# Performance work log

Hardware: AMD Instinct MI355X
Metric: run time of the kernel (lower is better)

The kernel has to match this reference:

```python
import jax, jax.numpy as jnp
import numpy as np

B, T, N, H = 256, 128, 128, 256  # batch, window, n_input_series, encoder hidden


def setup_inputs() -> dict:
    key = jax.random.key(0)
    ks = jax.random.split(key, 11)
    s = 0.05
    return {
        "input_data": jax.random.normal(ks[0], (B, T, N), jnp.float32),
        # attn_layer_hidden: Linear(2H -> T)
        "W_ah": jax.random.normal(ks[1], (T, 2 * H), jnp.float32) * s,
        "b_ah": jax.random.normal(ks[2], (T,), jnp.float32) * s,
        # attn_layer_input: Linear(T -> 1)
        "W_ai": jax.random.normal(ks[3], (1, T), jnp.float32) * s,
        "b_ai": jax.random.normal(ks[4], (1,), jnp.float32) * s,
        # attn_layer: Linear(T -> 1)
        "W_a": jax.random.normal(ks[5], (1, T), jnp.float32) * s,
        "b_a": jax.random.normal(ks[6], (1,), jnp.float32) * s,
        # LSTM(N -> H), gate order i,f,g,o (PyTorch)
        "W_ih": jax.random.normal(ks[7], (4 * H, N), jnp.float32) * s,
        "W_hh": jax.random.normal(ks[8], (4 * H, H), jnp.float32) * s,
        "b_ih": jax.random.normal(ks[9], (4 * H,), jnp.float32) * s,
        "b_hh": jax.random.normal(ks[10], (4 * H,), jnp.float32) * s,
    }


def reference(input_data, W_ah, b_ah, W_ai, b_ai, W_a, b_a, W_ih, W_hh, b_ih, b_hh):
    b, t_len, n = input_data.shape
    h_dim = W_hh.shape[1]
    dt = input_data.dtype

    # attn_layer_input part is time-invariant: [B, N] (one scalar per series)
    ipart = jnp.einsum('btn,t->bn', input_data, W_ai[0]) + b_ai[0]

    xs = jnp.swapaxes(input_data, 0, 1)  # [T, B, N]

    def step(carry, x_t):
        h, c = carry  # each [B, H]
        hc = jnp.concatenate([h, c], axis=-1)          # [B, 2H]
        hpart = hc @ W_ah.T + b_ah                      # [B, T]
        z = jnp.tanh(hpart[:, None, :] + ipart[:, :, None])  # [B, N, T]
        score = jnp.einsum('bnt,t->bn', z, W_a[0]) + b_a[0]   # [B, N]
        attn = jax.nn.softmax(score, axis=-1)
        wx = attn * x_t                                 # weighted input [B, N]
        gates = wx @ W_ih.T + b_ih + h @ W_hh.T + b_hh  # [B, 4H]
        i, f, g, o = jnp.split(gates, 4, axis=-1)
        i = jax.nn.sigmoid(i)
        f = jax.nn.sigmoid(f)
        g = jnp.tanh(g)
        o = jax.nn.sigmoid(o)
        c2 = f * c + i * g
        h2 = o * jnp.tanh(c2)
        return (h2, c2), (wx, h2)

    h0 = jnp.zeros((b, h_dim), dt)
    c0 = jnp.zeros((b, h_dim), dt)
    (_, _), (iw, ie) = jax.lax.scan(step, (h0, c0), xs)
    input_weighted = jnp.swapaxes(iw, 0, 1)  # [B, T, N]
    input_encoded = jnp.swapaxes(ie, 0, 1)   # [B, T, H]
    return input_weighted, input_encoded
```

## Files before the change

### kernel.cpp

```cpp
#include <hip/hip_runtime.h>
#include <cstdint>

#define NB 256
#define NT 128
#define NS 128
#define NH 256

#define NTHR 512
#define NWG  256
#define NGRP 64
#define GPW  4
#define GBAT 4
#define UPW  64

#define HC_OFF  0
#define CNT_OFF 131072

typedef _Float16 f16;
typedef _Float16 f16x2 __attribute__((ext_vector_type(2)));
typedef _Float16 f16x8 __attribute__((ext_vector_type(8)));
typedef float    f32x4 __attribute__((ext_vector_type(4)));

#define SAH 528
#define SAG 392

__device__ __forceinline__ f16x2 pk(float a, float b) {
  f16x2 r; r.x = (f16)a; r.y = (f16)b; return r;
}
__device__ __forceinline__ f16x8 pack8(const float* s) {
  float4 v0 = *(const float4*)s, v1 = *(const float4*)(s + 4);
  f16x8 r;
  r[0] = (f16)v0.x; r[1] = (f16)v0.y; r[2] = (f16)v0.z; r[3] = (f16)v0.w;
  r[4] = (f16)v1.x; r[5] = (f16)v1.y; r[6] = (f16)v1.z; r[7] = (f16)v1.w;
  return r;
}
__device__ __forceinline__ void awr(uint32_t* p, uint32_t v) {
  __hip_atomic_store(p, v, __ATOMIC_RELAXED, __HIP_MEMORY_SCOPE_AGENT);
}
__device__ __forceinline__ uint32_t ard(uint32_t* p) {
  return __hip_atomic_load(p, __ATOMIC_RELAXED, __HIP_MEMORY_SCOPE_AGENT);
}
__device__ __forceinline__ void cinc(uint32_t* p) {
  __hip_atomic_fetch_add(p, 1u, __ATOMIC_RELAXED, __HIP_MEMORY_SCOPE_AGENT);
}
__device__ __forceinline__ void cwait(uint32_t* p, uint32_t tgt) {
  while (ard(p) < tgt) __builtin_amdgcn_s_sleep(1);
}

struct __align__(16) Sm {
  f16   wahp[128 * SAH];
  f16   hcp[5 * SAH];
  f16   agxp[5 * SAG];
  float P[128 * 5];
  float scp[4 * 128];
  float gacc[256 * 4];
  float gbias[256];
  float cbuf[256];
  float w2a[128];
  float bah[128];
};

__global__ void enc_init(uint32_t* ws) {
  int i = blockIdx.x * blockDim.x + threadIdx.x;
  if (i < 65536) ws[HC_OFF + i] = 0u;
  if (i < 1024)  ws[CNT_OFF + i] = 0u;
}

__global__ __launch_bounds__(NTHR, 1) void enc_main(
    const float* __restrict__ x,    const float* __restrict__ W_ah,
    const float* __restrict__ b_ah, const float* __restrict__ W_ai,
    const float* __restrict__ b_ai, const float* __restrict__ W_a,
    const float* __restrict__ b_a,  const float* __restrict__ W_ih,
    const float* __restrict__ W_hh, const float* __restrict__ b_ih,
    const float* __restrict__ b_hh, float* __restrict__ out_iw,
    float* __restrict__ out_ie,     uint32_t* __restrict__ ws)
{
  __shared__ Sm sm;
  const int tid  = threadIdx.x;
  const int wg   = blockIdx.x;
  const int xcd  = wg & 7, slot = wg >> 3;
  const int g    = xcd * 8 + (slot >> 2);
  const int gid  = slot & 3;
  const int b0   = g * GBAT;
  const int u0   = gid * UPW;

  const int wv = tid >> 6, ln = tid & 63;
  const int bn = ln & 15, kq = ln >> 4;

  uint32_t* cnt = ws + CNT_OFF + g * 16;

  f16x8 wfrag[2][12];
  #pragma unroll
  for (int tt = 0; tt < 2; ++tt) {
    const int lr = wv * 32 + tt * 16 + bn;
    const int grow = (lr >> 6) * 256 + u0 + (lr & 63);
    #pragma unroll
    for (int kk = 0; kk < 4; ++kk)
      wfrag[tt][kk] = pack8(W_ih + (size_t)grow * NS + kk * 32 + kq * 8);
    #pragma unroll
    for (int kk = 4; kk < 12; ++kk)
      wfrag[tt][kk] = pack8(W_hh + (size_t)grow * NH + (kk - 4) * 32 + kq * 8);
  }

  #pragma unroll
  for (int i = 0; i < 16; ++i) {
    int idx = i * NTHR + tid;
    int r = idx >> 6, c = idx & 63;
    f16x8 v = pack8(W_ah + (size_t)r * 512 + c * 8);
    *(f16x8*)&sm.wahp[(size_t)r * SAH + c * 8] = v;
  }
  if (tid < 256) {
    int grow = (tid >> 6) * 256 + u0 + (tid & 63);
    sm.gbias[tid] = b_ih[grow] + b_hh[grow];
    sm.cbuf[tid] = 0.f;
  }
  if (tid < 128) { sm.w2a[tid] = 2.f * W_a[tid]; sm.bah[tid] = b_ah[tid]; }
  if (tid < 512) sm.hcp[4 * SAH + tid] = (f16)0.f;
  if (tid < 384) sm.agxp[4 * SAG + tid] = (f16)0.f;

  const int n_s = tid & 127, bq_s = tid >> 7;
  float ev;
  {
    const float* xb = x + (size_t)(b0 + bq_s) * NT * NS;
    float a = 0.f;
    #pragma unroll 4
    for (int t = 0; t < NT; ++t) a = fmaf(xb[(size_t)t * NS + n_s], W_ai[t], a);
    ev = __expf(2.f * (a + b_ai[0]));
  }
  float S0;
  { float s = b_a[0]; for (int i = 0; i < 128; ++i) s += W_a[i]; S0 = s; }

  __syncthreads();

  for (int t = 0; t < NT; ++t) {
    const int par = t & 1;
    float xv0 = 0.f, xv1 = 0.f;
    if (wv < 4) {
      const float* xr = x + ((size_t)(b0 + wv) * NT + t) * NS;
      xv0 = xr[ln]; xv1 = xr[ln + 64];
    }
    if (t > 0) {
      if (tid == 0) cwait(cnt, 4u * (uint32_t)t);
      __syncthreads();
    }
    {
      uint32_t* hcb = ws + HC_OFF + ((size_t)par * NGRP + g) * 1024;
      #pragma unroll
      for (int i = 0; i < 2; ++i) {
        int w = i * NTHR + tid;
        uint32_t v = ard(hcb + w);
        f16x2 pv = __builtin_bit_cast(f16x2, v);
        int b = w >> 8, u = w & 255;
        sm.hcp[b * SAH + u] = pv.x;
        sm.hcp[b * SAH + 256 + u] = pv.y;
        sm.agxp[b * SAG + 128 + u] = pv.x;
      }
    }
    __syncthreads();
    {
      f32x4 acc = {0.f, 0.f, 0.f, 0.f};
      const int br = (bn < 4) ? bn : 4;
      #pragma unroll
      for (int kk = 0; kk < 16; ++kk) {
        f16x8 a = *(const f16x8*)&sm.wahp[(size_t)(wv * 16 + bn) * SAH + kk * 32 + kq * 8];
        f16x8 b = *(const f16x8*)&sm.hcp[(size_t)br * SAH + kk * 32 + kq * 8];
        acc = __builtin_amdgcn_mfma_f32_16x16x32_f16(a, b, acc, 0, 0, 0);
      }
      if (bn < 4) {
        const int tp0 = wv * 16 + (ln >> 4) * 4;
        #pragma unroll
        for (int r = 0; r < 4; ++r)
          sm.P[(tp0 + r) * 5 + bn] = __expf(2.f * (acc[r] + sm.bah[tp0 + r]));
      }
    }
    __syncthreads();
    {
      float s = 0.f;
      #pragma unroll 8
      for (int tp = 0; tp < 128; ++tp) {
        float pe = fmaf(sm.P[tp * 5 + bq_s], ev, 1.f);
        s = fmaf(sm.w2a[tp], __builtin_amdgcn_rcpf(pe), s);
      }
      sm.scp[bq_s * 128 + n_s] = S0 - s;
    }
    __syncthreads();
    if (wv < 4) {
      float sA = sm.scp[wv * 128 + ln], sB = sm.scp[wv * 128 + ln + 64];
      float m = fmaxf(sA, sB);
      #pragma unroll
      for (int o = 32; o; o >>= 1) m = fmaxf(m, __shfl_xor(m, o));
      float eA = __expf(sA - m), eB = __expf(sB - m);
      float ss = eA + eB;
      #pragma unroll
      for (int o = 32; o; o >>= 1) ss += __shfl_xor(ss, o);
      float rs = 1.f / ss;
      float wxA = eA * rs * xv0, wxB = eB * rs * xv1;
      sm.agxp[wv * SAG + ln] = (f16)wxA;
      sm.agxp[wv * SAG + ln + 64] = (f16)wxB;
      if (wv == gid) {
        float* ow = out_iw + ((size_t)(b0 + wv) * NT + t) * NS;
        ow[ln] = wxA; ow[ln + 64] = wxB;
      }
    }
    __syncthreads();
    {
      const int br = (bn < 4) ? bn : 4;
      #pragma unroll
      for (int tt = 0; tt < 2; ++tt) {
        f32x4 acc = {0.f, 0.f, 0.f, 0.f};
        #pragma unroll
        for (int kk = 0; kk < 12; ++kk) {
          f16x8 a = *(const f16x8*)&sm.agxp[(size_t)br * SAG + kk * 32 + kq * 8];
          acc = __builtin_amdgcn_mfma_f32_16x16x32_f16(a, wfrag[tt][kk], acc, 0, 0, 0);
        }
        if (ln < 16)
          *(f32x4*)&sm.gacc[(wv * 32 + tt * 16 + ln) * 4] = acc;
      }
    }
    __syncthreads();
    if (tid < 256) {
      const int b = tid >> 6, ul = tid & 63;
      float gi = sm.gacc[(ul) * 4 + b]       + sm.gbias[ul];
      float gf = sm.gacc[(64 + ul) * 4 + b]  + sm.gbias[64 + ul];
      float gg = sm.gacc[(128 + ul) * 4 + b] + sm.gbias[128 + ul];
      float go = sm.gacc[(192 + ul) * 4 + b] + sm.gbias[192 + ul];
      float ii = 1.f / (1.f + __expf(-gi));
      float ff = 1.f / (1.f + __expf(-gf));
      float gt = 1.f - 2.f / (1.f + __expf(2.f * gg));
      float oo = 1.f / (1.f + __expf(-go));
      float c2 = ff * sm.cbuf[ul * 4 + b] + ii * gt;
      float h2 = oo * (1.f - 2.f / (1.f + __expf(2.f * c2)));
      sm.cbuf[ul * 4 + b] = c2;
      out_ie[((size_t)(b0 + b) * NT + t) * NH + u0 + ul] = h2;
      uint32_t* dst = ws + HC_OFF + ((size_t)(1 - par) * NGRP + g) * 1024 +
                      b * 256 + u0 + ul;
      awr(dst, __builtin_bit_cast(uint32_t, pk(h2, c2)));
    }
    __syncthreads();
    if (tid == 0) cinc(cnt);
  }
}

extern "C" void kernel_launch(void* const* d_in, const int* in_sizes, int n_in,
                              void* d_out, int out_size, void* d_ws, size_t ws_size,
                              hipStream_t stream) {
  const float* x    = (const float*)d_in[0];
  const float* W_ah = (const float*)d_in[1];
  const float* b_ah = (const float*)d_in[2];
  const float* W_ai = (const float*)d_in[3];
  const float* b_ai = (const float*)d_in[4];
  const float* W_a  = (const float*)d_in[5];
  const float* b_a  = (const float*)d_in[6];
  const float* W_ih = (const float*)d_in[7];
  const float* W_hh = (const float*)d_in[8];
  const float* b_ih = (const float*)d_in[9];
  const float* b_hh = (const float*)d_in[10];
  float* out_iw = (float*)d_out;
  float* out_ie = (float*)d_out + (size_t)NB * NT * NS;
  uint32_t* ws = (uint32_t*)d_ws;

  hipLaunchKernelGGL(enc_init, dim3(256), dim3(256), 0, stream, ws);
  hipLaunchKernelGGL(enc_main, dim3(NWG), dim3(NTHR), 0, stream,
                     x, W_ah, b_ah, W_ai, b_ai, W_a, b_a, W_ih, W_hh, b_ih, b_hh,
                     out_iw, out_ie, ws);
}
```

Baseline: 807.6 us.

## Double workgroup threads and split attention GEMM and score reduction across waves

Raises the block size from 512 to 1024 threads. The W_ah·hc MFMA is split into two K-halves with a separate reduction step, and the 128-term score loop is split across two thread halves whose partial sums are added before the softmax. Each wave now holds one gate-weight tile instead of two, which cuts register pressure. The aim is to shorten the per-timestep serial critical path of the recurrent loop, at the cost of an extra barrier and reduction stage per step. The launch_bounds change to (1024,4) also affects register allocation.

```diff
diff --git a/kernel.cpp b/kernel.cpp
--- a/kernel.cpp
+++ b/kernel.cpp
@@ -6,10 +6,9 @@
 #define NS 128
 #define NH 256
 
-#define NTHR 512
+#define NTHR 1024
 #define NWG  256
 #define NGRP 64
-#define GPW  4
 #define GBAT 4
 #define UPW  64
 
@@ -51,8 +50,11 @@
   f16   wahp[128 * SAH];
   f16   hcp[5 * SAH];
   f16   agxp[5 * SAG];
-  float P[128 * 5];
-  float scp[4 * 128];
+  float PW[128 * 5 * 2];
+  union {
+    float pacc[8][2][16][4];
+    float sp[2][4][128];
+  } u;
   float gacc[256 * 4];
   float gbias[256];
   float cbuf[256];
@@ -66,7 +68,7 @@
   if (i < 1024)  ws[CNT_OFF + i] = 0u;
 }
 
-__global__ __launch_bounds__(NTHR, 1) void enc_main(
+__global__ __launch_bounds__(NTHR, 4) void enc_main(
     const float* __restrict__ x,    const float* __restrict__ W_ah,
     const float* __restrict__ b_ah, const float* __restrict__ W_ai,
     const float* __restrict__ b_ai, const float* __restrict__ W_a,
@@ -89,21 +91,20 @@
 
   uint32_t* cnt = ws + CNT_OFF + g * 16;
 
-  f16x8 wfrag[2][12];
-  #pragma unroll
-  for (int tt = 0; tt < 2; ++tt) {
-    const int lr = wv * 32 + tt * 16 + bn;
+  f16x8 wfrag[12];
+  {
+    const int lr = wv * 16 + bn;
     const int grow = (lr >> 6) * 256 + u0 + (lr & 63);
     #pragma unroll
     for (int kk = 0; kk < 4; ++kk)
-      wfrag[tt][kk] = pack8(W_ih + (size_t)grow * NS + kk * 32 + kq * 8);
+      wfrag[kk] = pack8(W_ih + (size_t)grow * NS + kk * 32 + kq * 8);
     #pragma unroll
     for (int kk = 4; kk < 12; ++kk)
-      wfrag[tt][kk] = pack8(W_hh + (size_t)grow * NH + (kk - 4) * 32 + kq * 8);
+      wfrag[kk] = pack8(W_hh + (size_t)grow * NH + (kk - 4) * 32 + kq * 8);
   }
 
   #pragma unroll
-  for (int i = 0; i < 16; ++i) {
+  for (int i = 0; i < 8; ++i) {
     int idx = i * NTHR + tid;
     int r = idx >> 6, c = idx & 63;
     f16x8 v = pack8(W_ah + (size_t)r * 512 + c * 8);
@@ -118,7 +119,7 @@
   if (tid < 512) sm.hcp[4 * SAH + tid] = (f16)0.f;
   if (tid < 384) sm.agxp[4 * SAG + tid] = (f16)0.f;
 
-  const int n_s = tid & 127, bq_s = tid >> 7;
+  const int n_s = tid & 127, bq_s = (tid >> 7) & 3, ts_s = tid >> 9;
   float ev;
   {
     const float* xb = x + (size_t)(b0 + bq_s) * NT * NS;
@@ -145,47 +146,55 @@
     }
     {
       uint32_t* hcb = ws + HC_OFF + ((size_t)par * NGRP + g) * 1024;
-      #pragma unroll
-      for (int i = 0; i < 2; ++i) {
-        int w = i * NTHR + tid;
-        uint32_t v = ard(hcb + w);
-        f16x2 pv = __builtin_bit_cast(f16x2, v);
-        int b = w >> 8, u = w & 255;
-        sm.hcp[b * SAH + u] = pv.x;
-        sm.hcp[b * SAH + 256 + u] = pv.y;
-        sm.agxp[b * SAG + 128 + u] = pv.x;
-      }
-    }
-    __syncthreads();
-    {
+      uint32_t v = ard(hcb + tid);
+      f16x2 pv = __builtin_bit_cast(f16x2, v);
+      int b = tid >> 8, u = tid & 255;
+      sm.hcp[b * SAH + u] = pv.x;
+      sm.hcp[b * SAH + 256 + u] = pv.y;
+      sm.agxp[b * SAG + 128 + u] = pv.x;
+    }
+    __syncthreads();
+    {
+      const int tile = wv & 7, half = wv >> 3;
       f32x4 acc = {0.f, 0.f, 0.f, 0.f};
       const int br = (bn < 4) ? bn : 4;
       #pragma unroll
-      for (int kk = 0; kk < 16; ++kk) {
-        f16x8 a = *(const f16x8*)&sm.wahp[(size_t)(wv * 16 + bn) * SAH + kk * 32 + kq * 8];
+      for (int j = 0; j < 8; ++j) {
+        int kk = half * 8 + j;
+        f16x8 a = *(const f16x8*)&sm.wahp[(size_t)(tile * 16 + bn) * SAH + kk * 32 + kq * 8];
         f16x8 b = *(const f16x8*)&sm.hcp[(size_t)br * SAH + kk * 32 + kq * 8];
         acc = __builtin_amdgcn_mfma_f32_16x16x32_f16(a, b, acc, 0, 0, 0);
       }
       if (bn < 4) {
-        const int tp0 = wv * 16 + (ln >> 4) * 4;
         #pragma unroll
         for (int r = 0; r < 4; ++r)
-          sm.P[(tp0 + r) * 5 + bn] = __expf(2.f * (acc[r] + sm.bah[tp0 + r]));
-      }
+          sm.u.pacc[tile][half][kq * 4 + r][bn] = acc[r];
+      }
+    }
+    __syncthreads();
+    if (tid < 512) {
+      int tl = tid >> 2, b = tid & 3;
+      float p = sm.u.pacc[tl >> 4][0][tl & 15][b] + sm.u.pacc[tl >> 4][1][tl & 15][b];
+      float pe = __expf(2.f * (p + sm.bah[tl]));
+      sm.PW[(tl * 5 + b) * 2]     = pe;
+      sm.PW[(tl * 5 + b) * 2 + 1] = sm.w2a[tl];
     }
     __syncthreads();
     {
       float s = 0.f;
       #pragma unroll 8
-      for (int tp = 0; tp < 128; ++tp) {
-        float pe = fmaf(sm.P[tp * 5 + bq_s], ev, 1.f);
-        s = fmaf(sm.w2a[tp], __builtin_amdgcn_rcpf(pe), s);
-      }
-      sm.scp[bq_s * 128 + n_s] = S0 - s;
+      for (int i = 0; i < 64; ++i) {
+        int tp = ts_s * 64 + i;
+        float2 pw = *(const float2*)&sm.PW[(tp * 5 + bq_s) * 2];
+        float pe = fmaf(pw.x, ev, 1.f);
+        s = fmaf(pw.y, __builtin_amdgcn_rcpf(pe), s);
+      }
+      sm.u.sp[ts_s][bq_s][n_s] = s;
     }
     __syncthreads();
     if (wv < 4) {
-      float sA = sm.scp[wv * 128 + ln], sB = sm.scp[wv * 128 + ln + 64];
+      float sA = S0 - (sm.u.sp[0][wv][ln] + sm.u.sp[1][wv][ln]);
+      float sB = S0 - (sm.u.sp[0][wv][ln + 64] + sm.u.sp[1][wv][ln + 64]);
       float m = fmaxf(sA, sB);
       #pragma unroll
       for (int o = 32; o; o >>= 1) m = fmaxf(m, __shfl_xor(m, o));
@@ -205,17 +214,14 @@
     __syncthreads();
     {
       const int br = (bn < 4) ? bn : 4;
-      #pragma unroll
-      for (int tt = 0; tt < 2; ++tt) {
-        f32x4 acc = {0.f, 0.f, 0.f, 0.f};
-        #pragma unroll
-        for (int kk = 0; kk < 12; ++kk) {
-          f16x8 a = *(const f16x8*)&sm.agxp[(size_t)br * SAG + kk * 32 + kq * 8];
-          acc = __builtin_amdgcn_mfma_f32_16x16x32_f16(a, wfrag[tt][kk], acc, 0, 0, 0);
-        }
-        if (ln < 16)
-          *(f32x4*)&sm.gacc[(wv * 32 + tt * 16 + ln) * 4] = acc;
-      }
+      f32x4 acc = {0.f, 0.f, 0.f, 0.f};
+      #pragma unroll
+      for (int kk = 0; kk < 12; ++kk) {
+        f16x8 a = *(const f16x8*)&sm.agxp[(size_t)br * SAG + kk * 32 + kq * 8];
+        acc = __builtin_amdgcn_mfma_f32_16x16x32_f16(a, wfrag[kk], acc, 0, 0, 0);
+      }
+      if (ln < 16)
+        *(f32x4*)&sm.gacc[(wv * 16 + ln) * 4] = acc;
     }
     __syncthreads();
     if (tid < 256) {
```

Result: faster. 732.8 us (-9.3%).

## Repartition encoder into 2-batch groups of two 1024-thread workgroups

Applied to the files above, without the earlier changes.

Regroups the persistent LSTM encoder so each group handles 2 batch rows split across 2 workgroups of 1024 threads (128 hidden units each) instead of 4 rows across 4 workgroups of 512 threads. Each workgroup now keeps its own half of h/c in LDS and only reads the partner's half from global memory, which halves cross-workgroup traffic and the barrier fan-in. The score loop is split over 4 thread slices and pairs two reciprocals into one, with partial sums reduced afterwards. The cost is larger workgroups and more synchronising groups, and the MFMA tiles now hold 2 valid batch rows out of 16 instead of 4, so more of each tile is wasted.

```diff
diff --git a/kernel.cpp b/kernel.cpp
--- a/kernel.cpp
+++ b/kernel.cpp
@@ -5,13 +5,9 @@
 #define NT 128
 #define NS 128
 #define NH 256
-
-#define NTHR 512
+#define NTHR 1024
 #define NWG  256
-#define NGRP 64
-#define GPW  4
-#define GBAT 4
-#define UPW  64
+#define NGRP 128
 
 #define HC_OFF  0
 #define CNT_OFF 131072
@@ -21,8 +17,9 @@
 typedef _Float16 f16x8 __attribute__((ext_vector_type(8)));
 typedef float    f32x4 __attribute__((ext_vector_type(4)));
 
-#define SAH 528
-#define SAG 392
+#define SW 528
+#define SH 528
+#define SA 136
 
 __device__ __forceinline__ f16x2 pk(float a, float b) {
   f16x2 r; r.x = (f16)a; r.y = (f16)b; return r;
@@ -48,25 +45,24 @@
 }
 
 struct __align__(16) Sm {
-  f16   wahp[128 * SAH];
-  f16   hcp[5 * SAH];
-  f16   agxp[5 * SAG];
-  float P[128 * 5];
-  float scp[4 * 128];
-  float gacc[256 * 4];
-  float gbias[256];
-  float cbuf[256];
-  float w2a[128];
+  f16   wahp[128 * SW];
+  f16   hcp[3 * SH];
+  f16   act[3 * SA];
+  float PW[2 * 128 * 2];
+  float sp[4][2][128];
+  float gacc[512][2];
+  float gbias[512];
+  float cbuf[128 * 2];
   float bah[128];
 };
 
 __global__ void enc_init(uint32_t* ws) {
   int i = blockIdx.x * blockDim.x + threadIdx.x;
   if (i < 65536) ws[HC_OFF + i] = 0u;
-  if (i < 1024)  ws[CNT_OFF + i] = 0u;
-}
-
-__global__ __launch_bounds__(NTHR, 1) void enc_main(
+  if (i < 2048)  ws[CNT_OFF + i] = 0u;
+}
+
+__global__ __launch_bounds__(NTHR, 4) void enc_main(
     const float* __restrict__ x,    const float* __restrict__ W_ah,
     const float* __restrict__ b_ah, const float* __restrict__ W_ai,
     const float* __restrict__ b_ai, const float* __restrict__ W_a,
@@ -79,49 +75,55 @@
   const int tid  = threadIdx.x;
   const int wg   = blockIdx.x;
   const int xcd  = wg & 7, slot = wg >> 3;
-  const int g    = xcd * 8 + (slot >> 2);
-  const int gid  = slot & 3;
-  const int b0   = g * GBAT;
-  const int u0   = gid * UPW;
+  const int g    = xcd * 16 + (slot >> 1);
+  const int gid  = slot & 1;
+  const int b0   = g * 2;
+  const int u0   = gid * 128;
+  const int pu0  = 128 - u0;
 
   const int wv = tid >> 6, ln = tid & 63;
   const int bn = ln & 15, kq = ln >> 4;
-
-  uint32_t* cnt = ws + CNT_OFF + g * 16;
+  const int br2 = (bn < 2) ? bn : 2;
+
+  uint32_t* cnt = ws + CNT_OFF + (size_t)g * 16;
 
   f16x8 wfrag[2][12];
   #pragma unroll
-  for (int tt = 0; tt < 2; ++tt) {
-    const int lr = wv * 32 + tt * 16 + bn;
-    const int grow = (lr >> 6) * 256 + u0 + (lr & 63);
+  for (int s = 0; s < 2; ++s) {
+    const int lr = wv * 32 + s * 16 + bn;
+    const int grow = (lr >> 7) * 256 + u0 + (lr & 127);
     #pragma unroll
     for (int kk = 0; kk < 4; ++kk)
-      wfrag[tt][kk] = pack8(W_ih + (size_t)grow * NS + kk * 32 + kq * 8);
+      wfrag[s][kk] = pack8(W_ih + (size_t)grow * NS + kk * 32 + kq * 8);
     #pragma unroll
     for (int kk = 4; kk < 12; ++kk)
-      wfrag[tt][kk] = pack8(W_hh + (size_t)grow * NH + (kk - 4) * 32 + kq * 8);
+      wfrag[s][kk] = pack8(W_hh + (size_t)grow * NH + (kk - 4) * 32 + kq * 8);
   }
 
   #pragma unroll
-  for (int i = 0; i < 16; ++i) {
+  for (int i = 0; i < 8; ++i) {
     int idx = i * NTHR + tid;
     int r = idx >> 6, c = idx & 63;
     f16x8 v = pack8(W_ah + (size_t)r * 512 + c * 8);
-    *(f16x8*)&sm.wahp[(size_t)r * SAH + c * 8] = v;
+    *(f16x8*)&sm.wahp[(size_t)r * SW + c * 8] = v;
+  }
+  if (tid < 512) {
+    int grow = (tid >> 7) * 256 + u0 + (tid & 127);
+    sm.gbias[tid] = b_ih[grow] + b_hh[grow];
   }
   if (tid < 256) {
-    int grow = (tid >> 6) * 256 + u0 + (tid & 63);
-    sm.gbias[tid] = b_ih[grow] + b_hh[grow];
     sm.cbuf[tid] = 0.f;
-  }
-  if (tid < 128) { sm.w2a[tid] = 2.f * W_a[tid]; sm.bah[tid] = b_ah[tid]; }
-  if (tid < 512) sm.hcp[4 * SAH + tid] = (f16)0.f;
-  if (tid < 384) sm.agxp[4 * SAG + tid] = (f16)0.f;
-
-  const int n_s = tid & 127, bq_s = tid >> 7;
+    int b = tid >> 7, tp = tid & 127;
+    sm.PW[(b * 128 + tp) * 2 + 1] = 2.f * W_a[tp];
+  }
+  if (tid < 128) sm.bah[tid] = b_ah[tid];
+  for (int i = tid; i < 3 * SH; i += NTHR) sm.hcp[i] = (f16)0.f;
+  for (int i = tid; i < 3 * SA; i += NTHR) sm.act[i] = (f16)0.f;
+
+  const int n_s = tid & 127, b_s = (tid >> 7) & 1, ts_s = tid >> 8;
   float ev;
   {
-    const float* xb = x + (size_t)(b0 + bq_s) * NT * NS;
+    const float* xb = x + (size_t)(b0 + b_s) * NT * NS;
     float a = 0.f;
     #pragma unroll 4
     for (int t = 0; t < NT; ++t) a = fmaf(xb[(size_t)t * NS + n_s], W_ai[t], a);
@@ -133,59 +135,57 @@
   __syncthreads();
 
   for (int t = 0; t < NT; ++t) {
-    const int par = t & 1;
+    const int par = t & 1, par2 = 1 - par;
     float xv0 = 0.f, xv1 = 0.f;
-    if (wv < 4) {
+    if (wv < 2) {
       const float* xr = x + ((size_t)(b0 + wv) * NT + t) * NS;
       xv0 = xr[ln]; xv1 = xr[ln + 64];
     }
     if (t > 0) {
-      if (tid == 0) cwait(cnt, 4u * (uint32_t)t);
+      if (tid == 0) cwait(cnt, 2u * (uint32_t)t);
       __syncthreads();
-    }
-    {
-      uint32_t* hcb = ws + HC_OFF + ((size_t)par * NGRP + g) * 1024;
-      #pragma unroll
-      for (int i = 0; i < 2; ++i) {
-        int w = i * NTHR + tid;
-        uint32_t v = ard(hcb + w);
+      if (tid < 256) {
+        int b = tid >> 7, ul = tid & 127;
+        uint32_t v = ard(ws + HC_OFF + (((size_t)par * NGRP + g) * 2 + b) * 256 + pu0 + ul);
         f16x2 pv = __builtin_bit_cast(f16x2, v);
-        int b = w >> 8, u = w & 255;
-        sm.hcp[b * SAH + u] = pv.x;
-        sm.hcp[b * SAH + 256 + u] = pv.y;
-        sm.agxp[b * SAG + 128 + u] = pv.x;
-      }
-    }
-    __syncthreads();
-    {
+        sm.hcp[b * SH + pu0 + ul] = pv.x;
+        sm.hcp[b * SH + 256 + pu0 + ul] = pv.y;
+      }
+      __syncthreads();
+    }
+    if (wv < 8) {
       f32x4 acc = {0.f, 0.f, 0.f, 0.f};
-      const int br = (bn < 4) ? bn : 4;
       #pragma unroll
       for (int kk = 0; kk < 16; ++kk) {
-        f16x8 a = *(const f16x8*)&sm.wahp[(size_t)(wv * 16 + bn) * SAH + kk * 32 + kq * 8];
-        f16x8 b = *(const f16x8*)&sm.hcp[(size_t)br * SAH + kk * 32 + kq * 8];
+        f16x8 a = *(const f16x8*)&sm.wahp[(size_t)(wv * 16 + bn) * SW + kk * 32 + kq * 8];
+        f16x8 b = *(const f16x8*)&sm.hcp[(size_t)br2 * SH + kk * 32 + kq * 8];
         acc = __builtin_amdgcn_mfma_f32_16x16x32_f16(a, b, acc, 0, 0, 0);
       }
-      if (bn < 4) {
-        const int tp0 = wv * 16 + (ln >> 4) * 4;
+      if (bn < 2) {
         #pragma unroll
-        for (int r = 0; r < 4; ++r)
-          sm.P[(tp0 + r) * 5 + bn] = __expf(2.f * (acc[r] + sm.bah[tp0 + r]));
+        for (int r = 0; r < 4; ++r) {
+          int tp = wv * 16 + kq * 4 + r;
+          sm.PW[(bn * 128 + tp) * 2] = __expf(2.f * (acc[r] + sm.bah[tp]));
+        }
       }
     }
     __syncthreads();
     {
       float s = 0.f;
       #pragma unroll 8
-      for (int tp = 0; tp < 128; ++tp) {
-        float pe = fmaf(sm.P[tp * 5 + bq_s], ev, 1.f);
-        s = fmaf(sm.w2a[tp], __builtin_amdgcn_rcpf(pe), s);
-      }
-      sm.scp[bq_s * 128 + n_s] = S0 - s;
-    }
-    __syncthreads();
-    if (wv < 4) {
-      float sA = sm.scp[wv * 128 + ln], sB = sm.scp[wv * 128 + ln + 64];
+      for (int i = 0; i < 16; ++i) {
+        float4 rd = *(const float4*)&sm.PW[(b_s * 128 + ts_s * 32 + 2 * i) * 2];
+        float d1 = fmaf(rd.x, ev, 1.f);
+        float d2 = fmaf(rd.z, ev, 1.f);
+        float num = fmaf(rd.w, d1, rd.y * d2);
+        s = fmaf(num, __builtin_amdgcn_rcpf(d1 * d2), s);
+      }
+      sm.sp[ts_s][b_s][n_s] = s;
+    }
+    __syncthreads();
+    if (wv < 2) {
+      float sA = S0 - (sm.sp[0][wv][ln] + sm.sp[1][wv][ln] + sm.sp[2][wv][ln] + sm.sp[3][wv][ln]);
+      float sB = S0 - (sm.sp[0][wv][ln + 64] + sm.sp[1][wv][ln + 64] + sm.sp[2][wv][ln + 64] + sm.sp[3][wv][ln + 64]);
       float m = fmaxf(sA, sB);
       #pragma unroll
       for (int o = 32; o; o >>= 1) m = fmaxf(m, __shfl_xor(m, o));
@@ -195,46 +195,54 @@
       for (int o = 32; o; o >>= 1) ss += __shfl_xor(ss, o);
       float rs = 1.f / ss;
       float wxA = eA * rs * xv0, wxB = eB * rs * xv1;
-      sm.agxp[wv * SAG + ln] = (f16)wxA;
-      sm.agxp[wv * SAG + ln + 64] = (f16)wxB;
-      if (wv == gid) {
+      sm.act[wv * SA + ln] = (f16)wxA;
+      sm.act[wv * SA + ln + 64] = (f16)wxB;
+      if (gid == wv) {
         float* ow = out_iw + ((size_t)(b0 + wv) * NT + t) * NS;
         ow[ln] = wxA; ow[ln + 64] = wxB;
       }
     }
     __syncthreads();
     {
-      const int br = (bn < 4) ? bn : 4;
-      #pragma unroll
-      for (int tt = 0; tt < 2; ++tt) {
+      #pragma unroll
+      for (int s = 0; s < 2; ++s) {
         f32x4 acc = {0.f, 0.f, 0.f, 0.f};
         #pragma unroll
-        for (int kk = 0; kk < 12; ++kk) {
-          f16x8 a = *(const f16x8*)&sm.agxp[(size_t)br * SAG + kk * 32 + kq * 8];
-          acc = __builtin_amdgcn_mfma_f32_16x16x32_f16(a, wfrag[tt][kk], acc, 0, 0, 0);
-        }
-        if (ln < 16)
-          *(f32x4*)&sm.gacc[(wv * 32 + tt * 16 + ln) * 4] = acc;
+        for (int kk = 0; kk < 4; ++kk) {
+          f16x8 a = *(const f16x8*)&sm.act[(size_t)br2 * SA + kk * 32 + kq * 8];
+          acc = __builtin_amdgcn_mfma_f32_16x16x32_f16(a, wfrag[s][kk], acc, 0, 0, 0);
+        }
+        #pragma unroll
+        for (int kk = 4; kk < 12; ++kk) {
+          f16x8 a = *(const f16x8*)&sm.hcp[(size_t)br2 * SH + (kk - 4) * 32 + kq * 8];
+          acc = __builtin_amdgcn_mfma_f32_16x16x32_f16(a, wfrag[s][kk], acc, 0, 0, 0);
+        }
+        if (ln < 16) {
+          sm.gacc[wv * 32 + s * 16 + ln][0] = acc[0];
+          sm.gacc[wv * 32 + s * 16 + ln][1] = acc[1];
+        }
       }
     }
     __syncthreads();
     if (tid < 256) {
-      const int b = tid >> 6, ul = tid & 63;
-      float gi = sm.gacc[(ul) * 4 + b]       + sm.gbias[ul];
-      float gf = sm.gacc[(64 + ul) * 4 + b]  + sm.gbias[64 + ul];
-      float gg = sm.gacc[(128 + ul) * 4 + b] + sm.gbias[128 + ul];
-      float go = sm.gacc[(192 + ul) * 4 + b] + sm.gbias[192 + ul];
+      const int b = tid >> 7, ul = tid & 127;
+      float gi = sm.gacc[ul][b]        + sm.gbias[ul];
+      float gf = sm.gacc[128 + ul][b]  + sm.gbias[128 + ul];
+      float gg = sm.gacc[256 + ul][b]  + sm.gbias[256 + ul];
+      float go = sm.gacc[384 + ul][b]  + sm.gbias[384 + ul];
       float ii = 1.f / (1.f + __expf(-gi));
       float ff = 1.f / (1.f + __expf(-gf));
       float gt = 1.f - 2.f / (1.f + __expf(2.f * gg));
       float oo = 1.f / (1.f + __expf(-go));
-      float c2 = ff * sm.cbuf[ul * 4 + b] + ii * gt;
+      float c2 = ff * sm.cbuf[ul * 2 + b] + ii * gt;
       float h2 = oo * (1.f - 2.f / (1.f + __expf(2.f * c2)));
-      sm.cbuf[ul * 4 + b] = c2;
+      sm.cbuf[ul * 2 + b] = c2;
+      f16x2 pv = pk(h2, c2);
+      sm.hcp[b * SH + u0 + ul] = pv.x;
+      sm.hcp[b * SH + 256 + u0 + ul] = pv.y;
       out_ie[((size_t)(b0 + b) * NT + t) * NH + u0 + ul] = h2;
-      uint32_t* dst = ws + HC_OFF + ((size_t)(1 - par) * NGRP + g) * 1024 +
-                      b * 256 + u0 + ul;
-      awr(dst, __builtin_bit_cast(uint32_t, pk(h2, c2)));
+      awr(ws + HC_OFF + (((size_t)par2 * NGRP + g) * 2 + b) * 256 + u0 + ul,
+          __builtin_bit_cast(uint32_t, pv));
     }
     __syncthreads();
     if (tid == 0) cinc(cnt);
```

New measurement: 1.936 ms. 2.4x slower.
